# Kernel tuning notes

Measured on AMD Instinct MI355X. Metric: run time of the kernel, lower is better.

Reference implementation:

```python
import jax, jax.numpy as jnp
import numpy as np

HID, VOCAB, LAYERS, MAXLEN, SPAN = 1024, 32000, 4, 128, 2


def setup_inputs() -> dict:
    key = jax.random.key(0)
    ks = jax.random.split(key, 12)
    s = 0.02
    return {
        "input_ids": jax.random.randint(ks[0], (SPAN,), 0, VOCAB),
        "hidden": jax.random.normal(ks[1], (LAYERS, 1, HID), jnp.float32),
        "encoder_outputs": jax.random.normal(ks[2], (MAXLEN, HID), jnp.float32),
        "embedding": jax.random.normal(ks[3], (VOCAB, HID), jnp.float32) * s,
        "attn_W": jax.random.normal(ks[4], (MAXLEN, HID * (1 + SPAN)), jnp.float32) * s,
        "attn_b": jnp.zeros((MAXLEN,), jnp.float32),
        "comb_W": jax.random.normal(ks[5], (HID, HID * (1 + SPAN)), jnp.float32) * s,
        "comb_b": jnp.zeros((HID,), jnp.float32),
        "gru_Wih": jax.random.normal(ks[6], (LAYERS, 3 * HID, HID), jnp.float32) * s,
        "gru_Whh": jax.random.normal(ks[7], (LAYERS, 3 * HID, HID), jnp.float32) * s,
        "gru_bih": jnp.zeros((LAYERS, 3 * HID), jnp.float32),
        "gru_bhh": jnp.zeros((LAYERS, 3 * HID), jnp.float32),
        "out_W": jax.random.normal(ks[8], (VOCAB * SPAN, HID), jnp.float32) * s,
        "out_b": jnp.zeros((VOCAB * SPAN,), jnp.float32),
    }


def reference(input_ids, hidden, encoder_outputs, embedding, attn_W, attn_b,
              comb_W, comb_b, gru_Wih, gru_Whh, gru_bih, gru_bhh, out_W, out_b):
    # embed span tokens -> [1, SPAN*HID] (dropout = identity at eval)
    emb = embedding[input_ids].reshape(1, SPAN * HID)
    # attention over encoder outputs
    attn_in = jnp.concatenate([emb, hidden[0]], axis=1)          # [1, (1+SPAN)*HID]
    attn_weights = jax.nn.softmax(attn_in @ attn_W.T + attn_b, axis=1)  # [1, MAXLEN]
    attn_applied = attn_weights @ encoder_outputs                 # [1, HID]
    # combine + relu -> GRU input
    x = jax.nn.relu(jnp.concatenate([emb, attn_applied], axis=1) @ comb_W.T + comb_b)  # [1, HID]
    # multi-layer GRU single step (PyTorch gate order: r, z, n)
    new_h = []
    inp = x
    for l in range(LAYERS):
        h = hidden[l]                                             # [1, HID]
        gi = inp @ gru_Wih[l].T + gru_bih[l]                      # [1, 3*HID]
        gh = h @ gru_Whh[l].T + gru_bhh[l]
        i_r, i_z, i_n = jnp.split(gi, 3, axis=1)
        h_r, h_z, h_n = jnp.split(gh, 3, axis=1)
        r = jax.nn.sigmoid(i_r + h_r)
        z = jax.nn.sigmoid(i_z + h_z)
        n = jnp.tanh(i_n + r * h_n)
        h2 = (1.0 - z) * n + z * h
        new_h.append(h2)
        inp = h2
    hidden_new = jnp.stack(new_h)                                 # [LAYERS, 1, HID]
    # output projection, split into SPAN vocab chunks, log_softmax each
    logits = inp @ out_W.T + out_b                                # [1, SPAN*VOCAB]
    logp = jax.nn.log_softmax(logits.reshape(SPAN, VOCAB), axis=-1)  # [SPAN, VOCAB]
    return logp, hidden_new, attn_weights
```

## Files before the change

kernel.cpp:

```cpp
#include <hip/hip_runtime.h>
#include <math.h>

#define HID 1024
#define VOCAB 32000
#define LAYERS 4
#define MAXLEN 128
#define SPAN 2

#define OUT_LOGP 0
#define OUT_HID 64000
#define OUT_ATTNW 68096

#define WS_XCAT 0
#define WS_SCORES 3072
#define WS_X 3200
#define WS_GH 4224
#define WS_RED 16512
#define WS_LOGITS 24576

__device__ __forceinline__ float dot4(float4 a, float4 b) {
    return a.x * b.x + a.y * b.y + a.z * b.z + a.w * b.w;
}

__global__ __launch_bounds__(256) void k_pre(const int* __restrict__ ids,
                                             const float* __restrict__ hidden,
                                             const float* __restrict__ embedding,
                                             const float* __restrict__ attn_W,
                                             const float* __restrict__ attn_b,
                                             const float* __restrict__ gru_Whh,
                                             const float* __restrict__ gru_bhh,
                                             float* __restrict__ ws) {
    int b = blockIdx.x;
    int t = threadIdx.x;
    int lane = t & 63, wv = t >> 6;
    if (b < MAXLEN) {
        const float4* W4 = (const float4*)(attn_W + (size_t)b * 3072);
        float sum = 0.f;
#pragma unroll
        for (int i = 0; i < 3; i++) {
            int k4 = t + 256 * i;
            float4 w = W4[k4];
            int e = k4 * 4;
            float4 x;
            if (e < 2048) {
                int row = ids[e >> 10];
                x = *(const float4*)(embedding + (size_t)row * HID + (e & 1023));
            } else {
                x = *(const float4*)(hidden + (e - 2048));
            }
            sum += dot4(w, x);
        }
        __shared__ float sred[4];
        for (int o = 32; o > 0; o >>= 1) sum += __shfl_down(sum, o, 64);
        if (lane == 0) sred[wv] = sum;
        __syncthreads();
        if (t == 0) {
            float v = sred[0] + sred[1] + sred[2] + sred[3];
            ws[WS_SCORES + b] = v + attn_b[b];
        }
    } else if (b < MAXLEN + 8) {
        int idx = (b - MAXLEN) * 256 + t;
        int row = ids[idx >> 10];
        ws[WS_XCAT + idx] = embedding[(size_t)row * HID + (idx & 1023)];
    } else {
        int r = (b - MAXLEN - 8) * 4 + wv;
        int l = r / 3072;
        int g = r - l * 3072;
        const float4* W4 = (const float4*)(gru_Whh + ((size_t)l * 3072 + g) * HID);
        const float4* h4 = (const float4*)(hidden + (size_t)l * HID);
        float sum = 0.f;
#pragma unroll
        for (int i = 0; i < 4; i++) {
            int k4 = lane + 64 * i;
            sum += dot4(W4[k4], h4[k4]);
        }
        for (int o = 32; o > 0; o >>= 1) sum += __shfl_down(sum, o, 64);
        if (lane == 0) ws[WS_GH + r] = sum + gru_bhh[r];
    }
}

__global__ __launch_bounds__(256) void k_softmax_apply(const float* __restrict__ enc,
                                                       float* __restrict__ ws,
                                                       float* __restrict__ out) {
    __shared__ float w2[MAXLEN];
    __shared__ float part[8][32];
    int t = threadIdx.x;
    if (t < 128) w2[t] = ws[WS_SCORES + t];
    __syncthreads();
    float m = -INFINITY;
    for (int k = 0; k < 128; k++) m = fmaxf(m, w2[k]);
    float s = 0.f;
    for (int k = 0; k < 128; k++) s += expf(w2[k] - m);
    __syncthreads();
    if (t < 128) {
        float wt = expf(w2[t] - m) / s;
        if (blockIdx.x == 0) out[OUT_ATTNW + t] = wt;
        w2[t] = wt;
    }
    __syncthreads();
    int col = blockIdx.x * 32 + (t & 31);
    int seg = t >> 5;
    float p = 0.f;
#pragma unroll
    for (int k = 0; k < 16; k++)
        p += w2[seg * 16 + k] * enc[(size_t)(seg * 16 + k) * HID + col];
    part[seg][t & 31] = p;
    __syncthreads();
    if (t < 32) {
        float acc = 0.f;
#pragma unroll
        for (int s2 = 0; s2 < 8; s2++) acc += part[s2][t];
        ws[WS_XCAT + 2048 + blockIdx.x * 32 + t] = acc;
    }
}

__global__ __launch_bounds__(256) void k_comb(const float* __restrict__ comb_W,
                                              const float* __restrict__ comb_b,
                                              float* __restrict__ ws) {
    int r = blockIdx.x, t = threadIdx.x;
    const float4* W4 = (const float4*)(comb_W + (size_t)r * 3072);
    const float4* x4 = (const float4*)(ws + WS_XCAT);
    float sum = 0.f;
#pragma unroll
    for (int i = 0; i < 3; i++) {
        int k4 = t + 256 * i;
        sum += dot4(W4[k4], x4[k4]);
    }
    __shared__ float sred[4];
    int lane = t & 63, wid = t >> 6;
    for (int o = 32; o > 0; o >>= 1) sum += __shfl_down(sum, o, 64);
    if (lane == 0) sred[wid] = sum;
    __syncthreads();
    if (t == 0) {
        float v = sred[0] + sred[1] + sred[2] + sred[3];
        ws[WS_X + r] = fmaxf(v + comb_b[r], 0.f);
    }
}

__global__ __launch_bounds__(192) void k_gru(const float* __restrict__ inp,
                                             const float* __restrict__ h,
                                             const float* __restrict__ Wih,
                                             const float* __restrict__ bih,
                                             const float* __restrict__ gh,
                                             float* __restrict__ h_out) {
    int j = blockIdx.x;
    int t = threadIdx.x;
    int wv = t >> 6, lane = t & 63;
    __shared__ float dots[3];
    const float4* W4 = (const float4*)(Wih + ((size_t)wv * HID + j) * HID);
    const float4* x4 = (const float4*)inp;
    float sum = 0.f;
#pragma unroll
    for (int i = 0; i < 4; i++) {
        int k4 = lane + 64 * i;
        sum += dot4(W4[k4], x4[k4]);
    }
    for (int o = 32; o > 0; o >>= 1) sum += __shfl_down(sum, o, 64);
    if (lane == 0) dots[wv] = sum;
    __syncthreads();
    if (t == 0) {
        float ir = dots[0] + bih[j];
        float iz = dots[1] + bih[HID + j];
        float in_ = dots[2] + bih[2 * HID + j];
        float hr = gh[j];
        float hz = gh[HID + j];
        float hn = gh[2 * HID + j];
        float rg = 1.f / (1.f + expf(-(ir + hr)));
        float zg = 1.f / (1.f + expf(-(iz + hz)));
        float ng = tanhf(in_ + rg * hn);
        h_out[j] = (1.f - zg) * ng + zg * h[j];
    }
}

__global__ __launch_bounds__(256) void k_logits(const float* __restrict__ h3,
                                                const float* __restrict__ out_W,
                                                const float* __restrict__ out_b,
                                                float* __restrict__ ws) {
    int wv = threadIdx.x >> 6, lane = threadIdx.x & 63;
    int r0 = blockIdx.x * 32 + wv * 8;
    const float4* x4 = (const float4*)h3;
    float4 xv[4];
#pragma unroll
    for (int i = 0; i < 4; i++) xv[i] = x4[lane + 64 * i];
    const float4* W4 = (const float4*)(out_W + (size_t)r0 * HID);
    float s[8];
#pragma unroll
    for (int r = 0; r < 8; r++) {
        s[r] = 0.f;
#pragma unroll
        for (int k = 0; k < 4; k++)
            s[r] += dot4(W4[r * 256 + lane + 64 * k], xv[k]);
    }
#pragma unroll
    for (int r = 0; r < 8; r++)
        for (int o = 32; o > 0; o >>= 1) s[r] += __shfl_down(s[r], o, 64);
    __shared__ float sm[4], ss[4];
    if (lane == 0) {
        float4 b0 = *(const float4*)(out_b + r0);
        float4 b1 = *(const float4*)(out_b + r0 + 4);
        float v0 = s[0] + b0.x, v1 = s[1] + b0.y, v2 = s[2] + b0.z, v3 = s[3] + b0.w;
        float v4 = s[4] + b1.x, v5 = s[5] + b1.y, v6 = s[6] + b1.z, v7 = s[7] + b1.w;
        *(float4*)(ws + WS_LOGITS + r0) = make_float4(v0, v1, v2, v3);
        *(float4*)(ws + WS_LOGITS + r0 + 4) = make_float4(v4, v5, v6, v7);
        float vv[8] = {v0, v1, v2, v3, v4, v5, v6, v7};
        float M = vv[0], S = 1.f;
#pragma unroll
        for (int r = 1; r < 8; r++) {
            float v = vv[r];
            if (v > M) { S = S * expf(M - v) + 1.f; M = v; }
            else S += expf(v - M);
        }
        sm[wv] = M; ss[wv] = S;
    }
    __syncthreads();
    if (threadIdx.x == 0) {
        float M = sm[0], S = ss[0];
#pragma unroll
        for (int k = 1; k < 4; k++) {
            float mk = sm[k], sk = ss[k];
            if (mk > M) { S = S * expf(M - mk) + sk; M = mk; }
            else S += sk * expf(mk - M);
        }
        ws[WS_RED + blockIdx.x * 2] = M;
        ws[WS_RED + blockIdx.x * 2 + 1] = S;
    }
}

__global__ __launch_bounds__(256) void k_logp(const float* __restrict__ ws,
                                              float* __restrict__ out) {
    int t = threadIdx.x, b = blockIdx.x;
    int span = b / 125;
    int lane = t & 63, wv = t >> 6;
    __shared__ float sm[4], ss[4];
    __shared__ float gm_s, ls_s;
    float M = -INFINITY, S = 0.f;
#pragma unroll
    for (int k = 0; k < 4; k++) {
        int p = t + 256 * k;
        if (p < 1000) {
            float mk = ws[WS_RED + (span * 1000 + p) * 2];
            float sk = ws[WS_RED + (span * 1000 + p) * 2 + 1];
            if (mk > M) { S = S * expf(M - mk) + sk; M = mk; }
            else S += sk * expf(mk - M);
        }
    }
    for (int o = 32; o > 0; o >>= 1) {
        float Mo = __shfl_down(M, o, 64);
        float So = __shfl_down(S, o, 64);
        float nM = fmaxf(M, Mo);
        S = S * expf(M - nM) + So * expf(Mo - nM);
        M = nM;
    }
    if (lane == 0) { sm[wv] = M; ss[wv] = S; }
    __syncthreads();
    if (t == 0) {
        float Mf = sm[0], Sf = ss[0];
#pragma unroll
        for (int k = 1; k < 4; k++) {
            float mk = sm[k], sk = ss[k];
            if (mk > Mf) { Sf = Sf * expf(Mf - mk) + sk; Mf = mk; }
            else Sf += sk * expf(mk - Mf);
        }
        gm_s = Mf; ls_s = logf(Sf);
    }
    __syncthreads();
    int i = b * 256 + t;
    out[OUT_LOGP + i] = ws[WS_LOGITS + i] - gm_s - ls_s;
}

extern "C" void kernel_launch(void* const* d_in, const int* in_sizes, int n_in,
                              void* d_out, int out_size, void* d_ws, size_t ws_size,
                              hipStream_t stream) {
    const int* ids = (const int*)d_in[0];
    const float* hidden = (const float*)d_in[1];
    const float* enc = (const float*)d_in[2];
    const float* embedding = (const float*)d_in[3];
    const float* attn_W = (const float*)d_in[4];
    const float* attn_b = (const float*)d_in[5];
    const float* comb_W = (const float*)d_in[6];
    const float* comb_b = (const float*)d_in[7];
    const float* gru_Wih = (const float*)d_in[8];
    const float* gru_Whh = (const float*)d_in[9];
    const float* gru_bih = (const float*)d_in[10];
    const float* gru_bhh = (const float*)d_in[11];
    const float* out_W = (const float*)d_in[12];
    const float* out_b = (const float*)d_in[13];
    float* out = (float*)d_out;
    float* ws = (float*)d_ws;

    k_pre<<<3208, 256, 0, stream>>>(ids, hidden, embedding, attn_W, attn_b,
                                    gru_Whh, gru_bhh, ws);
    k_softmax_apply<<<32, 256, 0, stream>>>(enc, ws, out);
    k_comb<<<1024, 256, 0, stream>>>(comb_W, comb_b, ws);
    for (int l = 0; l < LAYERS; l++) {
        const float* inp = (l == 0) ? (ws + WS_X) : (out + OUT_HID + (l - 1) * HID);
        k_gru<<<1024, 192, 0, stream>>>(inp,
                                        hidden + (size_t)l * HID,
                                        gru_Wih + (size_t)l * 3 * HID * HID,
                                        gru_bih + (size_t)l * 3 * HID,
                                        ws + WS_GH + (size_t)l * 3 * HID,
                                        out + OUT_HID + l * HID);
    }
    k_logits<<<2000, 256, 0, stream>>>(out + OUT_HID + 3 * HID, out_W, out_b, ws);
    k_logp<<<250, 256, 0, stream>>>(ws, out);
}
```

Measured before the change: 511.1 us.

## Fuse all stages into one persistent kernel with software grid barriers

Replaces the nine separate kernel launches with one persistent 1024-block kernel that uses an atomic global barrier between stages (attention scores and Whh projections, softmax/apply, combine, four GRU layers, logits, log-softmax). This removes per-launch overhead and the idle gaps between dependent stages. The logits stage is also reorganised so each wave handles 16 rows with half-wave dot products. The design relies on all 1024 blocks being co-resident, and the barrier has a spin timeout that would silently break ordering if blocks cannot all be resident.

```diff
diff --git a/kernel.cpp b/kernel.cpp
--- a/kernel.cpp
+++ b/kernel.cpp
@@ -17,255 +17,297 @@
 #define WS_GH 4224
 #define WS_RED 16512
 #define WS_LOGITS 24576
+#define WS_BAR 88576
+
+#define NBLK 1024
 
 __device__ __forceinline__ float dot4(float4 a, float4 b) {
     return a.x * b.x + a.y * b.y + a.z * b.z + a.w * b.w;
 }
 
-__global__ __launch_bounds__(256) void k_pre(const int* __restrict__ ids,
-                                             const float* __restrict__ hidden,
-                                             const float* __restrict__ embedding,
-                                             const float* __restrict__ attn_W,
-                                             const float* __restrict__ attn_b,
-                                             const float* __restrict__ gru_Whh,
-                                             const float* __restrict__ gru_bhh,
-                                             float* __restrict__ ws) {
-    int b = blockIdx.x;
-    int t = threadIdx.x;
-    int lane = t & 63, wv = t >> 6;
-    if (b < MAXLEN) {
-        const float4* W4 = (const float4*)(attn_W + (size_t)b * 3072);
-        float sum = 0.f;
+__device__ __forceinline__ float wave_reduce(float s) {
+#pragma unroll
+    for (int o = 32; o > 0; o >>= 1) s += __shfl_down(s, o, 64);
+    return s;
+}
+
+__device__ __forceinline__ void gbar(unsigned* bar) {
+    __syncthreads();
+    if (threadIdx.x == 0) {
+        __threadfence();
+        unsigned gen = __hip_atomic_load(bar + 1, __ATOMIC_RELAXED,
+                                         __HIP_MEMORY_SCOPE_AGENT);
+        unsigned arrived = __hip_atomic_fetch_add(bar, 1u, __ATOMIC_ACQ_REL,
+                                                  __HIP_MEMORY_SCOPE_AGENT) + 1;
+        if (arrived == NBLK) {
+            __hip_atomic_store(bar, 0u, __ATOMIC_RELAXED,
+                               __HIP_MEMORY_SCOPE_AGENT);
+            __hip_atomic_fetch_add(bar + 1, 1u, __ATOMIC_RELEASE,
+                                   __HIP_MEMORY_SCOPE_AGENT);
+        } else {
+            unsigned spins = 0;
+            while (__hip_atomic_load(bar + 1, __ATOMIC_ACQUIRE,
+                                     __HIP_MEMORY_SCOPE_AGENT) == gen) {
+                __builtin_amdgcn_s_sleep(4);
+                if (++spins > (1u << 22)) break;
+            }
+        }
+        __threadfence();
+    }
+    __syncthreads();
+}
+
+__global__ __launch_bounds__(256, 4) void k_fused(
+    const int* __restrict__ ids,
+    const float* __restrict__ hidden,
+    const float* __restrict__ enc,
+    const float* __restrict__ embedding,
+    const float* __restrict__ attn_W,
+    const float* __restrict__ attn_b,
+    const float* __restrict__ comb_W,
+    const float* __restrict__ comb_b,
+    const float* __restrict__ gru_Wih,
+    const float* __restrict__ gru_Whh,
+    const float* __restrict__ gru_bih,
+    const float* __restrict__ gru_bhh,
+    const float* __restrict__ out_W,
+    const float* __restrict__ out_b,
+    float* __restrict__ out,
+    float* __restrict__ ws)
+{
+    unsigned* bar = (unsigned*)(ws + WS_BAR);
+    const int t = threadIdx.x;
+    const int lane = t & 63, wv = t >> 6;
+    const int blk = blockIdx.x;
+    const int gw = blk * 4 + wv;
+
+    __shared__ float sm8[4], ss8[4];
+    __shared__ float w2[MAXLEN];
+    __shared__ float part[8][32];
+    __shared__ float bc[2];
+    __shared__ float dred[3][4];
+
+    {
+#pragma unroll
+        for (int q = 0; q < 3; q++) {
+            int r = gw + 4096 * q;
+            int l = r / 3072;
+            const float4* W4 = (const float4*)(gru_Whh + (size_t)r * HID);
+            const float4* h4 = (const float4*)(hidden + (size_t)l * HID);
+            float s = 0.f;
+#pragma unroll
+            for (int i = 0; i < 4; i++) {
+                int k4 = lane + 64 * i;
+                s += dot4(W4[k4], h4[k4]);
+            }
+            s = wave_reduce(s);
+            if (lane == 0) ws[WS_GH + r] = s + gru_bhh[r];
+        }
+        if (gw < MAXLEN) {
+            int id0 = ids[0], id1 = ids[1];
+            const float4* W4 = (const float4*)(attn_W + (size_t)gw * 3072);
+            const float4* e0 = (const float4*)(embedding + (size_t)id0 * HID);
+            const float4* e1 = (const float4*)(embedding + (size_t)id1 * HID);
+            const float4* h0 = (const float4*)hidden;
+            float s = 0.f;
+#pragma unroll
+            for (int i = 0; i < 4; i++) { int k4 = lane + 64 * i; s += dot4(W4[k4], e0[k4]); }
+#pragma unroll
+            for (int i = 4; i < 8; i++) { int k4 = lane + 64 * i; s += dot4(W4[k4], e1[k4 - 256]); }
+#pragma unroll
+            for (int i = 8; i < 12; i++) { int k4 = lane + 64 * i; s += dot4(W4[k4], h0[k4 - 512]); }
+            s = wave_reduce(s);
+            if (lane == 0) ws[WS_SCORES + gw] = s + attn_b[gw];
+        }
+        if (blk >= 992 && blk < 1000) {
+            int idx = (blk - 992) * 256 + t;
+            int row = ids[idx >> 10];
+            ws[WS_XCAT + idx] = embedding[(size_t)row * HID + (idx & 1023)];
+        }
+    }
+    gbar(bar);
+
+    if (blk < 32) {
+        if (t < MAXLEN) w2[t] = ws[WS_SCORES + t];
+        __syncthreads();
+        float m = -INFINITY;
+        for (int k = 0; k < MAXLEN; k++) m = fmaxf(m, w2[k]);
+        float ssum = 0.f;
+        for (int k = 0; k < MAXLEN; k++) ssum += expf(w2[k] - m);
+        __syncthreads();
+        if (t < MAXLEN) {
+            float wt = expf(w2[t] - m) / ssum;
+            if (blk == 0) out[OUT_ATTNW + t] = wt;
+            w2[t] = wt;
+        }
+        __syncthreads();
+        int col = blk * 32 + (t & 31);
+        int seg = t >> 5;
+        float p = 0.f;
+#pragma unroll
+        for (int k = 0; k < 16; k++)
+            p += w2[seg * 16 + k] * enc[(size_t)(seg * 16 + k) * HID + col];
+        part[seg][t & 31] = p;
+        __syncthreads();
+        if (t < 32) {
+            float acc = 0.f;
+#pragma unroll
+            for (int s2 = 0; s2 < 8; s2++) acc += part[s2][t];
+            ws[WS_XCAT + 2048 + blk * 32 + t] = acc;
+        }
+    }
+    gbar(bar);
+
+    {
+        const float4* W4 = (const float4*)(comb_W + (size_t)blk * 3072);
+        const float4* x4 = (const float4*)(ws + WS_XCAT);
+        float s = 0.f;
 #pragma unroll
         for (int i = 0; i < 3; i++) {
             int k4 = t + 256 * i;
-            float4 w = W4[k4];
-            int e = k4 * 4;
-            float4 x;
-            if (e < 2048) {
-                int row = ids[e >> 10];
-                x = *(const float4*)(embedding + (size_t)row * HID + (e & 1023));
-            } else {
-                x = *(const float4*)(hidden + (e - 2048));
-            }
-            sum += dot4(w, x);
-        }
-        __shared__ float sred[4];
-        for (int o = 32; o > 0; o >>= 1) sum += __shfl_down(sum, o, 64);
-        if (lane == 0) sred[wv] = sum;
+            s += dot4(W4[k4], x4[k4]);
+        }
+        s = wave_reduce(s);
+        if (lane == 0) dred[0][wv] = s;
         __syncthreads();
         if (t == 0) {
-            float v = sred[0] + sred[1] + sred[2] + sred[3];
-            ws[WS_SCORES + b] = v + attn_b[b];
-        }
-    } else if (b < MAXLEN + 8) {
-        int idx = (b - MAXLEN) * 256 + t;
-        int row = ids[idx >> 10];
-        ws[WS_XCAT + idx] = embedding[(size_t)row * HID + (idx & 1023)];
-    } else {
-        int r = (b - MAXLEN - 8) * 4 + wv;
-        int l = r / 3072;
-        int g = r - l * 3072;
-        const float4* W4 = (const float4*)(gru_Whh + ((size_t)l * 3072 + g) * HID);
-        const float4* h4 = (const float4*)(hidden + (size_t)l * HID);
-        float sum = 0.f;
-#pragma unroll
-        for (int i = 0; i < 4; i++) {
-            int k4 = lane + 64 * i;
-            sum += dot4(W4[k4], h4[k4]);
-        }
-        for (int o = 32; o > 0; o >>= 1) sum += __shfl_down(sum, o, 64);
-        if (lane == 0) ws[WS_GH + r] = sum + gru_bhh[r];
-    }
-}
-
-__global__ __launch_bounds__(256) void k_softmax_apply(const float* __restrict__ enc,
-                                                       float* __restrict__ ws,
-                                                       float* __restrict__ out) {
-    __shared__ float w2[MAXLEN];
-    __shared__ float part[8][32];
-    int t = threadIdx.x;
-    if (t < 128) w2[t] = ws[WS_SCORES + t];
-    __syncthreads();
-    float m = -INFINITY;
-    for (int k = 0; k < 128; k++) m = fmaxf(m, w2[k]);
-    float s = 0.f;
-    for (int k = 0; k < 128; k++) s += expf(w2[k] - m);
-    __syncthreads();
-    if (t < 128) {
-        float wt = expf(w2[t] - m) / s;
-        if (blockIdx.x == 0) out[OUT_ATTNW + t] = wt;
-        w2[t] = wt;
-    }
-    __syncthreads();
-    int col = blockIdx.x * 32 + (t & 31);
-    int seg = t >> 5;
-    float p = 0.f;
-#pragma unroll
-    for (int k = 0; k < 16; k++)
-        p += w2[seg * 16 + k] * enc[(size_t)(seg * 16 + k) * HID + col];
-    part[seg][t & 31] = p;
-    __syncthreads();
-    if (t < 32) {
-        float acc = 0.f;
-#pragma unroll
-        for (int s2 = 0; s2 < 8; s2++) acc += part[s2][t];
-        ws[WS_XCAT + 2048 + blockIdx.x * 32 + t] = acc;
-    }
-}
-
-__global__ __launch_bounds__(256) void k_comb(const float* __restrict__ comb_W,
-                                              const float* __restrict__ comb_b,
-                                              float* __restrict__ ws) {
-    int r = blockIdx.x, t = threadIdx.x;
-    const float4* W4 = (const float4*)(comb_W + (size_t)r * 3072);
-    const float4* x4 = (const float4*)(ws + WS_XCAT);
-    float sum = 0.f;
-#pragma unroll
-    for (int i = 0; i < 3; i++) {
-        int k4 = t + 256 * i;
-        sum += dot4(W4[k4], x4[k4]);
-    }
-    __shared__ float sred[4];
-    int lane = t & 63, wid = t >> 6;
-    for (int o = 32; o > 0; o >>= 1) sum += __shfl_down(sum, o, 64);
-    if (lane == 0) sred[wid] = sum;
-    __syncthreads();
-    if (t == 0) {
-        float v = sred[0] + sred[1] + sred[2] + sred[3];
-        ws[WS_X + r] = fmaxf(v + comb_b[r], 0.f);
-    }
-}
-
-__global__ __launch_bounds__(192) void k_gru(const float* __restrict__ inp,
-                                             const float* __restrict__ h,
-                                             const float* __restrict__ Wih,
-                                             const float* __restrict__ bih,
-                                             const float* __restrict__ gh,
-                                             float* __restrict__ h_out) {
-    int j = blockIdx.x;
-    int t = threadIdx.x;
-    int wv = t >> 6, lane = t & 63;
-    __shared__ float dots[3];
-    const float4* W4 = (const float4*)(Wih + ((size_t)wv * HID + j) * HID);
-    const float4* x4 = (const float4*)inp;
-    float sum = 0.f;
-#pragma unroll
-    for (int i = 0; i < 4; i++) {
-        int k4 = lane + 64 * i;
-        sum += dot4(W4[k4], x4[k4]);
-    }
-    for (int o = 32; o > 0; o >>= 1) sum += __shfl_down(sum, o, 64);
-    if (lane == 0) dots[wv] = sum;
-    __syncthreads();
-    if (t == 0) {
-        float ir = dots[0] + bih[j];
-        float iz = dots[1] + bih[HID + j];
-        float in_ = dots[2] + bih[2 * HID + j];
-        float hr = gh[j];
-        float hz = gh[HID + j];
-        float hn = gh[2 * HID + j];
-        float rg = 1.f / (1.f + expf(-(ir + hr)));
-        float zg = 1.f / (1.f + expf(-(iz + hz)));
-        float ng = tanhf(in_ + rg * hn);
-        h_out[j] = (1.f - zg) * ng + zg * h[j];
-    }
-}
-
-__global__ __launch_bounds__(256) void k_logits(const float* __restrict__ h3,
-                                                const float* __restrict__ out_W,
-                                                const float* __restrict__ out_b,
-                                                float* __restrict__ ws) {
-    int wv = threadIdx.x >> 6, lane = threadIdx.x & 63;
-    int r0 = blockIdx.x * 32 + wv * 8;
-    const float4* x4 = (const float4*)h3;
-    float4 xv[4];
-#pragma unroll
-    for (int i = 0; i < 4; i++) xv[i] = x4[lane + 64 * i];
-    const float4* W4 = (const float4*)(out_W + (size_t)r0 * HID);
-    float s[8];
-#pragma unroll
-    for (int r = 0; r < 8; r++) {
-        s[r] = 0.f;
-#pragma unroll
-        for (int k = 0; k < 4; k++)
-            s[r] += dot4(W4[r * 256 + lane + 64 * k], xv[k]);
-    }
-#pragma unroll
-    for (int r = 0; r < 8; r++)
-        for (int o = 32; o > 0; o >>= 1) s[r] += __shfl_down(s[r], o, 64);
-    __shared__ float sm[4], ss[4];
-    if (lane == 0) {
-        float4 b0 = *(const float4*)(out_b + r0);
-        float4 b1 = *(const float4*)(out_b + r0 + 4);
-        float v0 = s[0] + b0.x, v1 = s[1] + b0.y, v2 = s[2] + b0.z, v3 = s[3] + b0.w;
-        float v4 = s[4] + b1.x, v5 = s[5] + b1.y, v6 = s[6] + b1.z, v7 = s[7] + b1.w;
-        *(float4*)(ws + WS_LOGITS + r0) = make_float4(v0, v1, v2, v3);
-        *(float4*)(ws + WS_LOGITS + r0 + 4) = make_float4(v4, v5, v6, v7);
-        float vv[8] = {v0, v1, v2, v3, v4, v5, v6, v7};
-        float M = vv[0], S = 1.f;
-#pragma unroll
-        for (int r = 1; r < 8; r++) {
-            float v = vv[r];
-            if (v > M) { S = S * expf(M - v) + 1.f; M = v; }
-            else S += expf(v - M);
-        }
-        sm[wv] = M; ss[wv] = S;
-    }
-    __syncthreads();
-    if (threadIdx.x == 0) {
-        float M = sm[0], S = ss[0];
-#pragma unroll
-        for (int k = 1; k < 4; k++) {
-            float mk = sm[k], sk = ss[k];
-            if (mk > M) { S = S * expf(M - mk) + sk; M = mk; }
-            else S += sk * expf(mk - M);
-        }
-        ws[WS_RED + blockIdx.x * 2] = M;
-        ws[WS_RED + blockIdx.x * 2 + 1] = S;
-    }
-}
-
-__global__ __launch_bounds__(256) void k_logp(const float* __restrict__ ws,
-                                              float* __restrict__ out) {
-    int t = threadIdx.x, b = blockIdx.x;
-    int span = b / 125;
-    int lane = t & 63, wv = t >> 6;
-    __shared__ float sm[4], ss[4];
-    __shared__ float gm_s, ls_s;
-    float M = -INFINITY, S = 0.f;
-#pragma unroll
-    for (int k = 0; k < 4; k++) {
-        int p = t + 256 * k;
-        if (p < 1000) {
-            float mk = ws[WS_RED + (span * 1000 + p) * 2];
-            float sk = ws[WS_RED + (span * 1000 + p) * 2 + 1];
-            if (mk > M) { S = S * expf(M - mk) + sk; M = mk; }
-            else S += sk * expf(mk - M);
-        }
-    }
-    for (int o = 32; o > 0; o >>= 1) {
-        float Mo = __shfl_down(M, o, 64);
-        float So = __shfl_down(S, o, 64);
-        float nM = fmaxf(M, Mo);
-        S = S * expf(M - nM) + So * expf(Mo - nM);
-        M = nM;
-    }
-    if (lane == 0) { sm[wv] = M; ss[wv] = S; }
-    __syncthreads();
-    if (t == 0) {
-        float Mf = sm[0], Sf = ss[0];
-#pragma unroll
-        for (int k = 1; k < 4; k++) {
-            float mk = sm[k], sk = ss[k];
-            if (mk > Mf) { Sf = Sf * expf(Mf - mk) + sk; Mf = mk; }
-            else Sf += sk * expf(mk - Mf);
-        }
-        gm_s = Mf; ls_s = logf(Sf);
-    }
-    __syncthreads();
-    int i = b * 256 + t;
-    out[OUT_LOGP + i] = ws[WS_LOGITS + i] - gm_s - ls_s;
+            float v = dred[0][0] + dred[0][1] + dred[0][2] + dred[0][3];
+            ws[WS_X + blk] = fmaxf(v + comb_b[blk], 0.f);
+        }
+    }
+    gbar(bar);
+
+    for (int l = 0; l < LAYERS; l++) {
+        {
+            int j = blk;
+            const float* inp = (l == 0) ? (ws + WS_X) : (out + OUT_HID + (l - 1) * HID);
+            const float4* x4 = (const float4*)inp;
+            int k4 = wv * 64 + lane;
+            float4 xv = x4[k4];
+            const float* Wl = gru_Wih + (size_t)l * 3 * HID * HID;
+            float s0 = dot4(((const float4*)(Wl + (size_t)j * HID))[k4], xv);
+            float s1 = dot4(((const float4*)(Wl + (size_t)(HID + j) * HID))[k4], xv);
+            float s2 = dot4(((const float4*)(Wl + (size_t)(2 * HID + j) * HID))[k4], xv);
+#pragma unroll
+            for (int o = 32; o > 0; o >>= 1) {
+                s0 += __shfl_down(s0, o, 64);
+                s1 += __shfl_down(s1, o, 64);
+                s2 += __shfl_down(s2, o, 64);
+            }
+            if (lane == 0) { dred[0][wv] = s0; dred[1][wv] = s1; dred[2][wv] = s2; }
+            __syncthreads();
+            if (t == 0) {
+                const float* bihl = gru_bih + (size_t)l * 3 * HID;
+                const float* ghl = ws + WS_GH + (size_t)l * 3 * HID;
+                float ir = dred[0][0] + dred[0][1] + dred[0][2] + dred[0][3] + bihl[j];
+                float iz = dred[1][0] + dred[1][1] + dred[1][2] + dred[1][3] + bihl[HID + j];
+                float in_ = dred[2][0] + dred[2][1] + dred[2][2] + dred[2][3] + bihl[2 * HID + j];
+                float rg = 1.f / (1.f + expf(-(ir + ghl[j])));
+                float zg = 1.f / (1.f + expf(-(iz + ghl[HID + j])));
+                float ng = tanhf(in_ + rg * ghl[2 * HID + j]);
+                out[OUT_HID + l * HID + j] =
+                    (1.f - zg) * ng + zg * hidden[(size_t)l * HID + j];
+            }
+        }
+        gbar(bar);
+    }
+
+    {
+        if (gw < 4000) {
+            const float* h3 = out + OUT_HID + 3 * HID;
+            const int half = lane >> 5;
+            const int l32 = lane & 31;
+            const float4* x4 = (const float4*)h3;
+            float4 xv[8];
+#pragma unroll
+            for (int i = 0; i < 8; i++) xv[i] = x4[l32 + 32 * i];
+            int r0 = gw * 16;
+            float s[8];
+#pragma unroll
+            for (int p = 0; p < 8; p++) {
+                int row = r0 + 2 * p + half;
+                const float4* W4 = (const float4*)(out_W + (size_t)row * HID);
+                float acc = 0.f;
+#pragma unroll
+                for (int i = 0; i < 8; i++) acc += dot4(W4[l32 + 32 * i], xv[i]);
+                s[p] = acc;
+            }
+#pragma unroll
+            for (int p = 0; p < 8; p++) {
+#pragma unroll
+                for (int o = 16; o > 0; o >>= 1) s[p] += __shfl_down(s[p], o, 32);
+            }
+            float M = -INFINITY, S = 0.f;
+            if (l32 == 0) {
+#pragma unroll
+                for (int p = 0; p < 8; p++) {
+                    int row = r0 + 2 * p + half;
+                    float v = s[p] + out_b[row];
+                    ws[WS_LOGITS + row] = v;
+                    if (v > M) { S = S * expf(M - v) + 1.f; M = v; }
+                    else S += expf(v - M);
+                }
+            }
+            float Mo = __shfl(M, 32, 64);
+            float So = __shfl(S, 32, 64);
+            if (lane == 0) {
+                float nM = fmaxf(M, Mo);
+                S = S * expf(M - nM) + So * expf(Mo - nM);
+                sm8[wv] = nM; ss8[wv] = S;
+            }
+        }
+        __syncthreads();
+        if (blk < 1000 && t == 0) {
+            float M = sm8[0], S = ss8[0];
+#pragma unroll
+            for (int k = 1; k < 4; k++) {
+                float mk = sm8[k], sk = ss8[k];
+                if (mk > M) { S = S * expf(M - mk) + sk; M = mk; }
+                else S += sk * expf(mk - M);
+            }
+            ws[WS_RED + blk * 2] = M;
+            ws[WS_RED + blk * 2 + 1] = S;
+        }
+    }
+    gbar(bar);
+
+    if (blk < 250) {
+        int span = blk / 125;
+        float M = -INFINITY, S = 0.f;
+#pragma unroll
+        for (int k = 0; k < 2; k++) {
+            int p = t + 256 * k;
+            if (p < 500) {
+                float mk = ws[WS_RED + (span * 500 + p) * 2];
+                float sk = ws[WS_RED + (span * 500 + p) * 2 + 1];
+                if (mk > M) { S = S * expf(M - mk) + sk; M = mk; }
+                else S += sk * expf(mk - M);
+            }
+        }
+#pragma unroll
+        for (int o = 32; o > 0; o >>= 1) {
+            float Mo = __shfl_down(M, o, 64);
+            float So = __shfl_down(S, o, 64);
+            float nM = fmaxf(M, Mo);
+            S = S * expf(M - nM) + So * expf(Mo - nM);
+            M = nM;
+        }
+        if (lane == 0) { sm8[wv] = M; ss8[wv] = S; }
+        __syncthreads();
+        if (t == 0) {
+            float Mf = sm8[0], Sf = ss8[0];
+#pragma unroll
+            for (int k = 1; k < 4; k++) {
+                float mk = sm8[k], sk = ss8[k];
+                if (mk > Mf) { Sf = Sf * expf(Mf - mk) + sk; Mf = mk; }
+                else Sf += sk * expf(mk - Mf);
+            }
+            bc[0] = Mf; bc[1] = logf(Sf);
+        }
+        __syncthreads();
+        int i = blk * 256 + t;
+        out[OUT_LOGP + i] = ws[WS_LOGITS + i] - bc[0] - bc[1];
+    }
 }
 
 extern "C" void kernel_launch(void* const* d_in, const int* in_sizes, int n_in,
@@ -288,19 +330,9 @@
     float* out = (float*)d_out;
     float* ws = (float*)d_ws;
 
-    k_pre<<<3208, 256, 0, stream>>>(ids, hidden, embedding, attn_W, attn_b,
-                                    gru_Whh, gru_bhh, ws);
-    k_softmax_apply<<<32, 256, 0, stream>>>(enc, ws, out);
-    k_comb<<<1024, 256, 0, stream>>>(comb_W, comb_b, ws);
-    for (int l = 0; l < LAYERS; l++) {
-        const float* inp = (l == 0) ? (ws + WS_X) : (out + OUT_HID + (l - 1) * HID);
-        k_gru<<<1024, 192, 0, stream>>>(inp,
-                                        hidden + (size_t)l * HID,
-                                        gru_Wih + (size_t)l * 3 * HID * HID,
-                                        gru_bih + (size_t)l * 3 * HID,
-                                        ws + WS_GH + (size_t)l * 3 * HID,
-                                        out + OUT_HID + l * HID);
-    }
-    k_logits<<<2000, 256, 0, stream>>>(out + OUT_HID + 3 * HID, out_W, out_b, ws);
-    k_logp<<<250, 256, 0, stream>>>(ws, out);
-}
+    hipMemsetAsync((char*)d_ws + (size_t)WS_BAR * 4, 0, 8, stream);
+
+    k_fused<<<NBLK, 256, 0, stream>>>(ids, hidden, enc, embedding, attn_W, attn_b,
+                                      comb_W, comb_b, gru_Wih, gru_Whh, gru_bih,
+                                      gru_bhh, out_W, out_b, out, ws);
+}
```

After: 1.701 ms. 3.33x slower.
